# Optimization experiments

Hardware: AMD Instinct MI355X
Metric: run time of the kernel (lower is better)

## Reference

```python
import jax, jax.numpy as jnp
import numpy as np

T, H, I, E, Z, TOPK = 1024, 1024, 512, 32, 8, 4
ROUTED_SCALING = 1.0


def setup_inputs() -> dict:
    key = jax.random.key(0)
    k1, k2, k3, k4 = jax.random.split(key, 4)
    return {
        "hidden_states": jax.random.normal(k1, (T, H), jnp.float32),
        "router_w": jax.random.normal(k2, (E + Z, H), jnp.float32) * 0.02,
        "correction_bias": jnp.zeros((E + Z,), jnp.float32),
        "w_gate_up": jax.random.normal(k3, (E, 2 * I, H), jnp.float32) * 0.02,
        "w_down": jax.random.normal(k4, (E, H, I), jnp.float32) * 0.02,
        "top_k": TOPK,
    }


def reference(hidden_states, router_w, correction_bias, w_gate_up, w_down, top_k):
    # hidden_states: [T, H]; router_w: [E+Z, H]; w_gate_up: [E, 2I, H]; w_down: [E, H, I]
    t, h = hidden_states.shape
    e = w_gate_up.shape[0]
    i = w_down.shape[2]
    # --- router (float32, no bias; correction bias only affects selection) ---
    logits = jnp.einsum("th,eh->te", hidden_states.astype(jnp.float32), router_w)
    scores = jax.nn.softmax(logits, axis=-1)                     # [T, E+Z]
    _, idx = jax.lax.top_k(scores + correction_bias[None, :], top_k)  # [T, k]
    w = jnp.take_along_axis(scores, idx, axis=1) * ROUTED_SCALING     # renormalize=False
    # combine matrix [T, E+Z] (sparse top-k scattered dense)
    comb = jnp.zeros((t, scores.shape[1]), jnp.float32)
    comb = comb.at[jnp.arange(t)[:, None], idx].add(w)
    comb_routed = comb[:, :e].astype(hidden_states.dtype)        # [T, E]
    zero_w = comb[:, e:].sum(-1).astype(hidden_states.dtype)     # [T] identity zero-experts
    # --- grouped SiLU-gated expert MLPs (dense all-experts reference) ---
    gu = jnp.einsum("th,eih->eti", hidden_states, w_gate_up)     # [E, T, 2I]
    hmid = jax.nn.silu(gu[..., :i]) * gu[..., i:]                # [E, T, I]
    ye = jnp.einsum("eti,ehi->eth", hmid, w_down)                # [E, T, H]
    out = jnp.einsum("te,eth->th", comb_routed, ye)
    out = out + zero_w[:, None] * hidden_states
    return out
```

## Files before the change

kernel.cpp:

```cpp
#include <hip/hip_runtime.h>
#include <hip/hip_bf16.h>
#include <math.h>

#define TT   1024
#define HH   1024
#define II   512
#define EE   32
#define NE   40
#define TOPK 4
#define CAP  1024

#define GM  128
#define GNP 16
#define GK  32
#define KP  40
#define DN  32

typedef __attribute__((ext_vector_type(4))) short short4v;
typedef __attribute__((ext_vector_type(8))) short short8v;
typedef __attribute__((ext_vector_type(4))) float floatx4;

static __device__ __forceinline__ short f2bf(float f) {
    unsigned u = __float_as_uint(f);
    unsigned r = (u + 0x7fffu + ((u >> 16) & 1u)) >> 16;
    return (short)(r & 0xffffu);
}
static __device__ __forceinline__ float bf2f(short s) {
    return __uint_as_float(((unsigned)(unsigned short)s) << 16);
}
#if defined(__has_builtin)
#if __has_builtin(__builtin_amdgcn_cvt_pk_bf16_f32)
#define HAVE_PK_BF16 1
#endif
#endif
static __device__ __forceinline__ unsigned pk2(float a, float b) {
#ifdef HAVE_PK_BF16
    typedef __attribute__((ext_vector_type(2))) __bf16 bf2t;
    union { bf2t v; unsigned u; } cv;
    cv.v = __builtin_amdgcn_cvt_pk_bf16_f32(a, b);
    return cv.u;
#else
    return (unsigned)(unsigned short)f2bf(a) | ((unsigned)(unsigned short)f2bf(b) << 16);
#endif
}
static __device__ __forceinline__ short4v cvt4(float4 v) {
    union { unsigned u[2]; short4v s; } cv;
    cv.u[0] = pk2(v.x, v.y); cv.u[1] = pk2(v.z, v.w);
    return cv.s;
}

struct SMem {
    short As[GM * KP];
    short Bs[2 * GNP * KP];
    int   sl[GM];
    float wvs[GM];
};


__global__ __launch_bounds__(256, 4) void kA(
    const float* __restrict__ x, const float* __restrict__ rw,
    const float* __restrict__ bias, float* __restrict__ topk_w,
    float* __restrict__ zero_w, int* __restrict__ kexp,
    int* __restrict__ counts, int* __restrict__ slots, short* __restrict__ xb)
{
    const int bx = blockIdx.x, tid = threadIdx.x;
    const int lane = tid & 63;
    const int w    = tid >> 6;

    if (w < 2) {
        const int t = bx * 2 + w;
        float xv[16];
        #pragma unroll
        for (int i = 0; i < 16; ++i) xv[i] = x[(size_t)t * HH + 64 * i + lane];

        float mylogit = -INFINITY;
        for (int e0 = 0; e0 < NE; e0 += 4) {
            const float* r0 = rw + (size_t)e0 * HH;
            float p[4] = { 0.f, 0.f, 0.f, 0.f };
            #pragma unroll
            for (int i = 0; i < 16; ++i) {
                int h = 64 * i + lane;
                #pragma unroll
                for (int j = 0; j < 4; ++j) p[j] += xv[i] * r0[(size_t)j * HH + h];
            }
            #pragma unroll
            for (int j = 0; j < 4; ++j) {
                #pragma unroll
                for (int off = 32; off > 0; off >>= 1) p[j] += __shfl_xor(p[j], off);
                if (lane == e0 + j) mylogit = p[j];
            }
        }

        float m = mylogit;
        #pragma unroll
        for (int off = 32; off > 0; off >>= 1) m = fmaxf(m, __shfl_xor(m, off));
        float pexp = (lane < NE) ? expf(mylogit - m) : 0.f;
        float s = pexp;
        #pragma unroll
        for (int off = 32; off > 0; off >>= 1) s += __shfl_xor(s, off);
        const float score = pexp / s;

        float val = (lane < NE) ? score + bias[lane] : -INFINITY;
        int   kidx[TOPK];
        float kw[TOPK];
        #pragma unroll
        for (int k = 0; k < TOPK; ++k) {
            float v = val; int idx = lane;
            #pragma unroll
            for (int off = 32; off > 0; off >>= 1) {
                float ov = __shfl_xor(v, off);
                int   oi = __shfl_xor(idx, off);
                if (ov > v || (ov == v && oi < idx)) { v = ov; idx = oi; }
            }
            kidx[k] = idx;
            kw[k]   = __shfl(score, idx);
            if (lane == idx) val = -INFINITY;
        }

        if (lane == 0) {
            float zw = 0.f;
            #pragma unroll
            for (int k = 0; k < TOPK; ++k) {
                int slot = t * TOPK + k;
                topk_w[slot] = kw[k];
                kexp[slot]   = kidx[k];
                if (kidx[k] < EE) {
                    int pos = atomicAdd(&counts[kidx[k]], 1);
                    slots[kidx[k] * CAP + pos] = slot;
                } else {
                    zw += kw[k];
                }
            }
            zero_w[t] = zw;
        }
    } else {
        const int t = bx * 2 + (w - 2);
        const float4* xr = (const float4*)(x + (size_t)t * HH);
        short4v* xbr = (short4v*)(xb + (size_t)t * HH);
        #pragma unroll
        for (int i = 0; i < 4; ++i) xbr[lane + 64 * i] = cvt4(xr[lane + 64 * i]);
    }
}

__global__ __launch_bounds__(256, 4) void kB(
    const short* __restrict__ xb, const float* __restrict__ wgu,
    const int* __restrict__ counts, const int* __restrict__ slots,
    const float* __restrict__ topk_w, short* __restrict__ hmid)
{
    __shared__ SMem sm;
    const int bx = blockIdx.x, tid = threadIdx.x;
    const int e      = bx >> 5;
    const int c_base = (bx & 31) * GNP;
    const int cnt    = counts[e];
    const float* wb  = wgu + (size_t)e * (2 * II) * HH;

    const int lane = tid & 63;
    const int w    = tid >> 6;
    const int quad = lane >> 4;
    const int mcol = lane & 15;

    for (int m_base = 0; m_base < cnt; m_base += GM) {
        if (tid < GM) {
            int m = m_base + tid;
            int s = (m < cnt) ? slots[e * CAP + m] : -1;
            sm.sl[tid]  = s;
            sm.wvs[tid] = (s >= 0) ? topk_w[s] : 0.f;
        }
        __syncthreads();

        const int kcA = tid & 3;
        int rowA[2]; int slA[2]; const short* pA[2];
        #pragma unroll
        for (int it = 0; it < 2; ++it) {
            rowA[it] = (tid >> 2) + 64 * it;
            int s = sm.sl[rowA[it]];
            slA[it] = s;
            pA[it] = xb + (size_t)((s >= 0 ? s : 0) >> 2) * HH + kcA * 8;
        }
        const int kq   = tid & 7;
        const int rowB = tid >> 3;
        const int grow = (rowB < GNP) ? (c_base + rowB)
                                      : (II + c_base + (rowB - GNP));
        const float* pB = wb + (size_t)grow * HH + kq * 4;

        floatx4 accg[2] = {};
        floatx4 accu[2] = {};
        short8v pa[2]; float4 pb;
        const short8v szv = { 0,0,0,0,0,0,0,0 };

        #pragma unroll
        for (int it = 0; it < 2; ++it) pa[it] = (slA[it] >= 0) ? *(const short8v*)(pA[it]) : szv;
        pb = *(const float4*)(pB);

        for (int k0 = 0; k0 < HH; k0 += GK) {
            #pragma unroll
            for (int it = 0; it < 2; ++it) *(short8v*)&sm.As[rowA[it] * KP + kcA * 8] = pa[it];
            *(short4v*)&sm.Bs[rowB * KP + kq * 4] = cvt4(pb);
            __syncthreads();

            const int kn = k0 + GK;
            if (kn < HH) {
                #pragma unroll
                for (int it = 0; it < 2; ++it) pa[it] = (slA[it] >= 0) ? *(const short8v*)(pA[it] + kn) : szv;
                pb = *(const float4*)(pB + kn);
            }

            short8v a[2], bg, bu;
            #pragma unroll
            for (int i = 0; i < 2; ++i)
                a[i] = *(const short8v*)&sm.As[(w * 32 + i * 16 + mcol) * KP + quad * 8];
            bg = *(const short8v*)&sm.Bs[(mcol) * KP + quad * 8];
            bu = *(const short8v*)&sm.Bs[(GNP + mcol) * KP + quad * 8];
            #pragma unroll
            for (int i = 0; i < 2; ++i) {
                accg[i] = __builtin_amdgcn_mfma_f32_16x16x32_bf16(a[i], bg, accg[i], 0, 0, 0);
                accu[i] = __builtin_amdgcn_mfma_f32_16x16x32_bf16(a[i], bu, accu[i], 0, 0, 0);
            }
            __syncthreads();
        }

        #pragma unroll
        for (int i = 0; i < 2; ++i) {
            #pragma unroll
            for (int r = 0; r < 4; ++r) {
                int m = w * 32 + i * 16 + quad * 4 + r;
                int s = sm.sl[m];
                if (s < 0) continue;
                float g = accg[i][r], u = accu[i][r];
                float valf = sm.wvs[m] * g * u / (1.f + __expf(-g));
                hmid[(size_t)s * II + c_base + mcol] = f2bf(valf);
            }
        }
        __syncthreads();
    }
}

__global__ __launch_bounds__(256, 4) void kC(
    const short* __restrict__ hmid, const float* __restrict__ wd,
    const int* __restrict__ counts, const int* __restrict__ slots,
    short* __restrict__ ydown)
{
    __shared__ SMem sm;
    const int bx = blockIdx.x, tid = threadIdx.x;
    const int e      = bx >> 5;
    const int n_base = (bx & 31) * DN;
    const int cnt    = counts[e];
    const float* wb  = wd + (size_t)e * HH * II;

    const int lane = tid & 63;
    const int w    = tid >> 6;
    const int quad = lane >> 4;
    const int mcol = lane & 15;

    for (int m_base = 0; m_base < cnt; m_base += GM) {
        if (tid < GM) {
            int m = m_base + tid;
            sm.sl[tid] = (m < cnt) ? slots[e * CAP + m] : -1;
        }
        __syncthreads();

        const int kcA = tid & 3;
        int rowA[2]; int slA[2]; const short* pA[2];
        #pragma unroll
        for (int it = 0; it < 2; ++it) {
            rowA[it] = (tid >> 2) + 64 * it;
            int s = sm.sl[rowA[it]];
            slA[it] = s;
            pA[it] = hmid + (size_t)(s >= 0 ? s : 0) * II + kcA * 8;
        }
        const int kq   = tid & 7;
        const int rowB = tid >> 3;
        const float* pB = wb + (size_t)(n_base + rowB) * II + kq * 4;

        floatx4 acc[2][2] = {};
        short8v pa[2]; float4 pb;
        const short8v szv = { 0,0,0,0,0,0,0,0 };

        #pragma unroll
        for (int it = 0; it < 2; ++it) pa[it] = (slA[it] >= 0) ? *(const short8v*)(pA[it]) : szv;
        pb = *(const float4*)(pB);

        for (int k0 = 0; k0 < II; k0 += GK) {
            #pragma unroll
            for (int it = 0; it < 2; ++it) *(short8v*)&sm.As[rowA[it] * KP + kcA * 8] = pa[it];
            *(short4v*)&sm.Bs[rowB * KP + kq * 4] = cvt4(pb);
            __syncthreads();

            const int kn = k0 + GK;
            if (kn < II) {
                #pragma unroll
                for (int it = 0; it < 2; ++it) pa[it] = (slA[it] >= 0) ? *(const short8v*)(pA[it] + kn) : szv;
                pb = *(const float4*)(pB + kn);
            }

            short8v a[2], b[2];
            #pragma unroll
            for (int i = 0; i < 2; ++i)
                a[i] = *(const short8v*)&sm.As[(w * 32 + i * 16 + mcol) * KP + quad * 8];
            #pragma unroll
            for (int j = 0; j < 2; ++j)
                b[j] = *(const short8v*)&sm.Bs[(j * 16 + mcol) * KP + quad * 8];
            #pragma unroll
            for (int i = 0; i < 2; ++i)
                #pragma unroll
                for (int j = 0; j < 2; ++j)
                    acc[i][j] = __builtin_amdgcn_mfma_f32_16x16x32_bf16(a[i], b[j], acc[i][j], 0, 0, 0);
            __syncthreads();
        }

        #pragma unroll
        for (int i = 0; i < 2; ++i) {
            #pragma unroll
            for (int r = 0; r < 4; ++r) {
                int m = w * 32 + i * 16 + quad * 4 + r;
                int s = sm.sl[m];
                if (s < 0) continue;
                short* yrow = ydown + (size_t)s * HH + n_base;
                #pragma unroll
                for (int j = 0; j < 2; ++j)
                    yrow[j * 16 + mcol] = f2bf(acc[i][j][r]);
            }
        }
        __syncthreads();
    }
}

__global__ __launch_bounds__(256, 4) void kD(
    const float* __restrict__ x, const short* __restrict__ ydown,
    const int* __restrict__ kexp, const float* __restrict__ zero_w,
    float* __restrict__ out)
{
    const int bx = blockIdx.x, tid = threadIdx.x;
    const int t = bx;
    const float4 xvv = ((const float4*)(x + (size_t)t * HH))[tid];
    const float zw = zero_w[t];
    float4 o;
    o.x = zw * xvv.x; o.y = zw * xvv.y; o.z = zw * xvv.z; o.w = zw * xvv.w;
    #pragma unroll
    for (int k = 0; k < TOPK; ++k) {
        int slot = t * TOPK + k;
        if (kexp[slot] < EE) {
            short4v y = *(const short4v*)&ydown[(size_t)slot * HH + tid * 4];
            o.x += bf2f(y[0]); o.y += bf2f(y[1]);
            o.z += bf2f(y[2]); o.w += bf2f(y[3]);
        }
    }
    ((float4*)(out + (size_t)t * HH))[tid] = o;
}

extern "C" void kernel_launch(void* const* d_in, const int* in_sizes, int n_in,
                              void* d_out, int out_size, void* d_ws, size_t ws_size,
                              hipStream_t stream) {
    const float* x    = (const float*)d_in[0];
    const float* rw   = (const float*)d_in[1];
    const float* bias = (const float*)d_in[2];
    const float* wgu  = (const float*)d_in[3];
    const float* wd   = (const float*)d_in[4];
    float* out = (float*)d_out;

    char* ws = (char*)d_ws;
    int*   counts = (int*)ws;
    float* topk_w = (float*)(ws + 1024);
    float* zero_w = (float*)(ws + 17408);
    int*   kexp   = (int*)(ws + 21504);
    int*   slots  = (int*)(ws + 40960);
    short* xb     = (short*)(ws + 262144);
    short* hmid   = (short*)(ws + 2359296);
    short* ydown  = (short*)(ws + 6553600);

    hipMemsetAsync(counts, 0, EE * sizeof(int), stream);

    kA<<<dim3(512),  dim3(256), 0, stream>>>(x, rw, bias, topk_w, zero_w, kexp, counts, slots, xb);
    kB<<<dim3(1024), dim3(256), 0, stream>>>(xb, wgu, counts, slots, topk_w, hmid);
    kC<<<dim3(1024), dim3(256), 0, stream>>>(hmid, wd, counts, slots, ydown);
    kD<<<dim3(1024), dim3(256), 0, stream>>>(x, ydown, kexp, zero_w, out);
}
```

Before: 319.6 us.

## Load MFMA operands directly from global into registers and build slots deterministically

```diff
diff --git a/kernel.cpp b/kernel.cpp
--- a/kernel.cpp
+++ b/kernel.cpp
@@ -11,10 +11,7 @@
 #define CAP  1024
 
 #define GM  128
-#define GNP 16
 #define GK  32
-#define KP  40
-#define DN  32
 
 typedef __attribute__((ext_vector_type(4))) short short4v;
 typedef __attribute__((ext_vector_type(8))) short short8v;
@@ -48,20 +45,18 @@
     cv.u[0] = pk2(v.x, v.y); cv.u[1] = pk2(v.z, v.w);
     return cv.s;
 }
-
-struct SMem {
-    short As[GM * KP];
-    short Bs[2 * GNP * KP];
-    int   sl[GM];
-    float wvs[GM];
-};
+static __device__ __forceinline__ short8v pack8(float4 f0, float4 f1) {
+    union { short4v h[2]; short8v v; } u;
+    u.h[0] = cvt4(f0); u.h[1] = cvt4(f1);
+    return u.v;
+}
 
 
 __global__ __launch_bounds__(256, 4) void kA(
     const float* __restrict__ x, const float* __restrict__ rw,
     const float* __restrict__ bias, float* __restrict__ topk_w,
     float* __restrict__ zero_w, int* __restrict__ kexp,
-    int* __restrict__ counts, int* __restrict__ slots, short* __restrict__ xb)
+    short* __restrict__ xb)
 {
     const int bx = blockIdx.x, tid = threadIdx.x;
     const int lane = tid & 63;
@@ -124,12 +119,7 @@
                 int slot = t * TOPK + k;
                 topk_w[slot] = kw[k];
                 kexp[slot]   = kidx[k];
-                if (kidx[k] < EE) {
-                    int pos = atomicAdd(&counts[kidx[k]], 1);
-                    slots[kidx[k] * CAP + pos] = slot;
-                } else {
-                    zw += kw[k];
-                }
+                if (kidx[k] >= EE) zw += kw[k];
             }
             zero_w[t] = zw;
         }
@@ -142,15 +132,46 @@
     }
 }
 
-__global__ __launch_bounds__(256, 4) void kB(
+__global__ __launch_bounds__(256, 4) void kA2(
+    const int* __restrict__ kexp, int* __restrict__ counts,
+    int* __restrict__ slots)
+{
+    __shared__ int wsum[4];
+    __shared__ int base;
+    const int e = blockIdx.x;
+    const int tid = threadIdx.x, lane = tid & 63, w = tid >> 6;
+    if (tid == 0) base = 0;
+    __syncthreads();
+    for (int i0 = 0; i0 < TT * TOPK; i0 += 256) {
+        const int i = i0 + tid;
+        const bool m = (kexp[i] == e);
+        unsigned long long bal = __ballot(m);
+        int pre  = __popcll(bal & ((1ull << lane) - 1ull));
+        int wcnt = __popcll(bal);
+        if (lane == 0) wsum[w] = wcnt;
+        __syncthreads();
+        int woff = 0;
+        #pragma unroll
+        for (int j = 0; j < 4; ++j) if (j < w) woff += wsum[j];
+        const int tot = wsum[0] + wsum[1] + wsum[2] + wsum[3];
+        if (m) slots[e * CAP + base + woff + pre] = i;
+        __syncthreads();
+        if (tid == 0) base += tot;
+        __syncthreads();
+    }
+    if (tid == 0) counts[e] = base;
+}
+
+__global__ __launch_bounds__(256, 3) void kB(
     const short* __restrict__ xb, const float* __restrict__ wgu,
     const int* __restrict__ counts, const int* __restrict__ slots,
     const float* __restrict__ topk_w, short* __restrict__ hmid)
 {
-    __shared__ SMem sm;
+    __shared__ int   ssl[GM];
+    __shared__ float swv[GM];
     const int bx = blockIdx.x, tid = threadIdx.x;
     const int e      = bx >> 5;
-    const int c_base = (bx & 31) * GNP;
+    const int c_base = (bx & 31) * 16;
     const int cnt    = counts[e];
     const float* wb  = wgu + (size_t)e * (2 * II) * HH;
 
@@ -158,92 +179,134 @@
     const int w    = tid >> 6;
     const int quad = lane >> 4;
     const int mcol = lane & 15;
+    constexpr int NSLAB = HH / GK;
+
+    const float* pG = wb + (size_t)(c_base + mcol) * HH + quad * 8;
+    const float* pU = wb + (size_t)(II + c_base + mcol) * HH + quad * 8;
 
     for (int m_base = 0; m_base < cnt; m_base += GM) {
+        __syncthreads();
         if (tid < GM) {
             int m = m_base + tid;
             int s = (m < cnt) ? slots[e * CAP + m] : -1;
-            sm.sl[tid]  = s;
-            sm.wvs[tid] = (s >= 0) ? topk_w[s] : 0.f;
-        }
-        __syncthreads();
-
-        const int kcA = tid & 3;
-        int rowA[2]; int slA[2]; const short* pA[2];
-        #pragma unroll
-        for (int it = 0; it < 2; ++it) {
-            rowA[it] = (tid >> 2) + 64 * it;
-            int s = sm.sl[rowA[it]];
-            slA[it] = s;
-            pA[it] = xb + (size_t)((s >= 0 ? s : 0) >> 2) * HH + kcA * 8;
-        }
-        const int kq   = tid & 7;
-        const int rowB = tid >> 3;
-        const int grow = (rowB < GNP) ? (c_base + rowB)
-                                      : (II + c_base + (rowB - GNP));
-        const float* pB = wb + (size_t)grow * HH + kq * 4;
-
-        floatx4 accg[2] = {};
-        floatx4 accu[2] = {};
-        short8v pa[2]; float4 pb;
-        const short8v szv = { 0,0,0,0,0,0,0,0 };
-
-        #pragma unroll
-        for (int it = 0; it < 2; ++it) pa[it] = (slA[it] >= 0) ? *(const short8v*)(pA[it]) : szv;
-        pb = *(const float4*)(pB);
-
-        for (int k0 = 0; k0 < HH; k0 += GK) {
-            #pragma unroll
-            for (int it = 0; it < 2; ++it) *(short8v*)&sm.As[rowA[it] * KP + kcA * 8] = pa[it];
-            *(short4v*)&sm.Bs[rowB * KP + kq * 4] = cvt4(pb);
-            __syncthreads();
-
-            const int kn = k0 + GK;
-            if (kn < HH) {
-                #pragma unroll
-                for (int it = 0; it < 2; ++it) pa[it] = (slA[it] >= 0) ? *(const short8v*)(pA[it] + kn) : szv;
-                pb = *(const float4*)(pB + kn);
-            }
-
-            short8v a[2], bg, bu;
-            #pragma unroll
-            for (int i = 0; i < 2; ++i)
-                a[i] = *(const short8v*)&sm.As[(w * 32 + i * 16 + mcol) * KP + quad * 8];
-            bg = *(const short8v*)&sm.Bs[(mcol) * KP + quad * 8];
-            bu = *(const short8v*)&sm.Bs[(GNP + mcol) * KP + quad * 8];
-            #pragma unroll
-            for (int i = 0; i < 2; ++i) {
-                accg[i] = __builtin_amdgcn_mfma_f32_16x16x32_bf16(a[i], bg, accg[i], 0, 0, 0);
-                accu[i] = __builtin_amdgcn_mfma_f32_16x16x32_bf16(a[i], bu, accu[i], 0, 0, 0);
-            }
-            __syncthreads();
-        }
-
-        #pragma unroll
-        for (int i = 0; i < 2; ++i) {
-            #pragma unroll
-            for (int r = 0; r < 4; ++r) {
-                int m = w * 32 + i * 16 + quad * 4 + r;
-                int s = sm.sl[m];
-                if (s < 0) continue;
-                float g = accg[i][r], u = accu[i][r];
-                float valf = sm.wvs[m] * g * u / (1.f + __expf(-g));
-                hmid[(size_t)s * II + c_base + mcol] = f2bf(valf);
-            }
-        }
-        __syncthreads();
+            ssl[tid] = s;
+            swv[tid] = (s >= 0) ? topk_w[s] : 0.f;
+        }
+        __syncthreads();
+
+        const short *pA0, *pA1;
+        {
+            int s0 = ssl[w * 32 +      mcol];
+            int s1 = ssl[w * 32 + 16 + mcol];
+            pA0 = xb + (size_t)((s0 >= 0 ? s0 : 0) >> 2) * HH + quad * 8;
+            pA1 = xb + (size_t)((s1 >= 0 ? s1 : 0) >> 2) * HH + quad * 8;
+        }
+
+        floatx4 accg0 = {}, accg1 = {}, accu0 = {}, accu1 = {};
+
+        float4 g0_0,g1_0,u0_0,u1_0, g0_1,g1_1,u0_1,u1_1,
+               g0_2,g1_2,u0_2,u1_2, g0_3,g1_3,u0_3,u1_3;
+        short8v a0_0,a1_0, a0_1,a1_1;
+
+        g0_0=*(const float4*)(pG       ); g1_0=*(const float4*)(pG+4       );
+        u0_0=*(const float4*)(pU       ); u1_0=*(const float4*)(pU+4       );
+        g0_1=*(const float4*)(pG+GK    ); g1_1=*(const float4*)(pG+GK+4    );
+        u0_1=*(const float4*)(pU+GK    ); u1_1=*(const float4*)(pU+GK+4    );
+        g0_2=*(const float4*)(pG+2*GK  ); g1_2=*(const float4*)(pG+2*GK+4  );
+        u0_2=*(const float4*)(pU+2*GK  ); u1_2=*(const float4*)(pU+2*GK+4  );
+        g0_3=*(const float4*)(pG+3*GK  ); g1_3=*(const float4*)(pG+3*GK+4  );
+        u0_3=*(const float4*)(pU+3*GK  ); u1_3=*(const float4*)(pU+3*GK+4  );
+        a0_0=*(const short8v*)(pA0     ); a1_0=*(const short8v*)(pA1     );
+        a0_1=*(const short8v*)(pA0+GK  ); a1_1=*(const short8v*)(pA1+GK  );
+
+        for (int t = 0; t < NSLAB; t += 4) {
+            {
+                short8v bg = pack8(g0_0,g1_0), bu = pack8(u0_0,u1_0);
+                accg0 = __builtin_amdgcn_mfma_f32_16x16x32_bf16(a0_0, bg, accg0, 0, 0, 0);
+                accu0 = __builtin_amdgcn_mfma_f32_16x16x32_bf16(a0_0, bu, accu0, 0, 0, 0);
+                accg1 = __builtin_amdgcn_mfma_f32_16x16x32_bf16(a1_0, bg, accg1, 0, 0, 0);
+                accu1 = __builtin_amdgcn_mfma_f32_16x16x32_bf16(a1_0, bu, accu1, 0, 0, 0);
+                const int kb_ = (t + 4) * GK;
+                if (kb_ < HH) {
+                    g0_0=*(const float4*)(pG+kb_); g1_0=*(const float4*)(pG+kb_+4);
+                    u0_0=*(const float4*)(pU+kb_); u1_0=*(const float4*)(pU+kb_+4);
+                }
+                const int ka_ = (t + 2) * GK;
+                if (ka_ < HH) { a0_0=*(const short8v*)(pA0+ka_); a1_0=*(const short8v*)(pA1+ka_); }
+            }
+            {
+                short8v bg = pack8(g0_1,g1_1), bu = pack8(u0_1,u1_1);
+                accg0 = __builtin_amdgcn_mfma_f32_16x16x32_bf16(a0_1, bg, accg0, 0, 0, 0);
+                accu0 = __builtin_amdgcn_mfma_f32_16x16x32_bf16(a0_1, bu, accu0, 0, 0, 0);
+                accg1 = __builtin_amdgcn_mfma_f32_16x16x32_bf16(a1_1, bg, accg1, 0, 0, 0);
+                accu1 = __builtin_amdgcn_mfma_f32_16x16x32_bf16(a1_1, bu, accu1, 0, 0, 0);
+                const int kb_ = (t + 5) * GK;
+                if (kb_ < HH) {
+                    g0_1=*(const float4*)(pG+kb_); g1_1=*(const float4*)(pG+kb_+4);
+                    u0_1=*(const float4*)(pU+kb_); u1_1=*(const float4*)(pU+kb_+4);
+                }
+                const int ka_ = (t + 3) * GK;
+                if (ka_ < HH) { a0_1=*(const short8v*)(pA0+ka_); a1_1=*(const short8v*)(pA1+ka_); }
+            }
+            {
+                short8v bg = pack8(g0_2,g1_2), bu = pack8(u0_2,u1_2);
+                accg0 = __builtin_amdgcn_mfma_f32_16x16x32_bf16(a0_0, bg, accg0, 0, 0, 0);
+                accu0 = __builtin_amdgcn_mfma_f32_16x16x32_bf16(a0_0, bu, accu0, 0, 0, 0);
+                accg1 = __builtin_amdgcn_mfma_f32_16x16x32_bf16(a1_0, bg, accg1, 0, 0, 0);
+                accu1 = __builtin_amdgcn_mfma_f32_16x16x32_bf16(a1_0, bu, accu1, 0, 0, 0);
+                const int kb_ = (t + 6) * GK;
+                if (kb_ < HH) {
+                    g0_2=*(const float4*)(pG+kb_); g1_2=*(const float4*)(pG+kb_+4);
+                    u0_2=*(const float4*)(pU+kb_); u1_2=*(const float4*)(pU+kb_+4);
+                }
+                const int ka_ = (t + 4) * GK;
+                if (ka_ < HH) { a0_0=*(const short8v*)(pA0+ka_); a1_0=*(const short8v*)(pA1+ka_); }
+            }
+            {
+                short8v bg = pack8(g0_3,g1_3), bu = pack8(u0_3,u1_3);
+                accg0 = __builtin_amdgcn_mfma_f32_16x16x32_bf16(a0_1, bg, accg0, 0, 0, 0);
+                accu0 = __builtin_amdgcn_mfma_f32_16x16x32_bf16(a0_1, bu, accu0, 0, 0, 0);
+                accg1 = __builtin_amdgcn_mfma_f32_16x16x32_bf16(a1_1, bg, accg1, 0, 0, 0);
+                accu1 = __builtin_amdgcn_mfma_f32_16x16x32_bf16(a1_1, bu, accu1, 0, 0, 0);
+                const int kb_ = (t + 7) * GK;
+                if (kb_ < HH) {
+                    g0_3=*(const float4*)(pG+kb_); g1_3=*(const float4*)(pG+kb_+4);
+                    u0_3=*(const float4*)(pU+kb_); u1_3=*(const float4*)(pU+kb_+4);
+                }
+                const int ka_ = (t + 5) * GK;
+                if (ka_ < HH) { a0_1=*(const short8v*)(pA0+ka_); a1_1=*(const short8v*)(pA1+ka_); }
+            }
+        }
+
+        #pragma unroll
+        for (int r = 0; r < 4; ++r) {
+            int m0 = w * 32 + quad * 4 + r;
+            int s0 = ssl[m0];
+            if (s0 >= 0) {
+                float g = accg0[r], u = accu0[r];
+                hmid[(size_t)s0 * II + c_base + mcol] =
+                    f2bf(swv[m0] * g * u / (1.f + __expf(-g)));
+            }
+            int m1 = w * 32 + 16 + quad * 4 + r;
+            int s1 = ssl[m1];
+            if (s1 >= 0) {
+                float g = accg1[r], u = accu1[r];
+                hmid[(size_t)s1 * II + c_base + mcol] =
+                    f2bf(swv[m1] * g * u / (1.f + __expf(-g)));
+            }
+        }
     }
 }
 
-__global__ __launch_bounds__(256, 4) void kC(
+__global__ __launch_bounds__(256, 3) void kC(
     const short* __restrict__ hmid, const float* __restrict__ wd,
     const int* __restrict__ counts, const int* __restrict__ slots,
     short* __restrict__ ydown)
 {
-    __shared__ SMem sm;
+    __shared__ int ssl[GM];
     const int bx = blockIdx.x, tid = threadIdx.x;
     const int e      = bx >> 5;
-    const int n_base = (bx & 31) * DN;
+    const int n_base = (bx & 31) * 32;
     const int cnt    = counts[e];
     const float* wb  = wd + (size_t)e * HH * II;
 
@@ -251,77 +314,120 @@
     const int w    = tid >> 6;
     const int quad = lane >> 4;
     const int mcol = lane & 15;
+    constexpr int NSLAB = II / GK;
+
+    const float* pW0 = wb + (size_t)(n_base +      mcol) * II + quad * 8;
+    const float* pW1 = wb + (size_t)(n_base + 16 + mcol) * II + quad * 8;
 
     for (int m_base = 0; m_base < cnt; m_base += GM) {
+        __syncthreads();
         if (tid < GM) {
             int m = m_base + tid;
-            sm.sl[tid] = (m < cnt) ? slots[e * CAP + m] : -1;
-        }
-        __syncthreads();
-
-        const int kcA = tid & 3;
-        int rowA[2]; int slA[2]; const short* pA[2];
-        #pragma unroll
-        for (int it = 0; it < 2; ++it) {
-            rowA[it] = (tid >> 2) + 64 * it;
-            int s = sm.sl[rowA[it]];
-            slA[it] = s;
-            pA[it] = hmid + (size_t)(s >= 0 ? s : 0) * II + kcA * 8;
-        }
-        const int kq   = tid & 7;
-        const int rowB = tid >> 3;
-        const float* pB = wb + (size_t)(n_base + rowB) * II + kq * 4;
-
-        floatx4 acc[2][2] = {};
-        short8v pa[2]; float4 pb;
-        const short8v szv = { 0,0,0,0,0,0,0,0 };
-
-        #pragma unroll
-        for (int it = 0; it < 2; ++it) pa[it] = (slA[it] >= 0) ? *(const short8v*)(pA[it]) : szv;
-        pb = *(const float4*)(pB);
-
-        for (int k0 = 0; k0 < II; k0 += GK) {
-            #pragma unroll
-            for (int it = 0; it < 2; ++it) *(short8v*)&sm.As[rowA[it] * KP + kcA * 8] = pa[it];
-            *(short4v*)&sm.Bs[rowB * KP + kq * 4] = cvt4(pb);
-            __syncthreads();
-
-            const int kn = k0 + GK;
-            if (kn < II) {
-                #pragma unroll
-                for (int it = 0; it < 2; ++it) pa[it] = (slA[it] >= 0) ? *(const short8v*)(pA[it] + kn) : szv;
-                pb = *(const float4*)(pB + kn);
-            }
-
-            short8v a[2], b[2];
-            #pragma unroll
-            for (int i = 0; i < 2; ++i)
-                a[i] = *(const short8v*)&sm.As[(w * 32 + i * 16 + mcol) * KP + quad * 8];
-            #pragma unroll
-            for (int j = 0; j < 2; ++j)
-                b[j] = *(const short8v*)&sm.Bs[(j * 16 + mcol) * KP + quad * 8];
-            #pragma unroll
-            for (int i = 0; i < 2; ++i)
-                #pragma unroll
-                for (int j = 0; j < 2; ++j)
-                    acc[i][j] = __builtin_amdgcn_mfma_f32_16x16x32_bf16(a[i], b[j], acc[i][j], 0, 0, 0);
-            __syncthreads();
-        }
-
-        #pragma unroll
-        for (int i = 0; i < 2; ++i) {
-            #pragma unroll
-            for (int r = 0; r < 4; ++r) {
-                int m = w * 32 + i * 16 + quad * 4 + r;
-                int s = sm.sl[m];
-                if (s < 0) continue;
-                short* yrow = ydown + (size_t)s * HH + n_base;
-                #pragma unroll
-                for (int j = 0; j < 2; ++j)
-                    yrow[j * 16 + mcol] = f2bf(acc[i][j][r]);
-            }
-        }
-        __syncthreads();
+            ssl[tid] = (m < cnt) ? slots[e * CAP + m] : -1;
+        }
+        __syncthreads();
+
+        const short *pA0, *pA1;
+        {
+            int s0 = ssl[w * 32 +      mcol];
+            int s1 = ssl[w * 32 + 16 + mcol];
+            pA0 = hmid + (size_t)(s0 >= 0 ? s0 : 0) * II + quad * 8;
+            pA1 = hmid + (size_t)(s1 >= 0 ? s1 : 0) * II + quad * 8;
+        }
+
+        floatx4 acc00 = {}, acc01 = {}, acc10 = {}, acc11 = {};
+
+        float4 p0_0,p1_0,q0_0,q1_0, p0_1,p1_1,q0_1,q1_1,
+               p0_2,p1_2,q0_2,q1_2, p0_3,p1_3,q0_3,q1_3;
+        short8v a0_0,a1_0, a0_1,a1_1;
+
+        p0_0=*(const float4*)(pW0      ); p1_0=*(const float4*)(pW0+4      );
+        q0_0=*(const float4*)(pW1      ); q1_0=*(const float4*)(pW1+4      );
+        p0_1=*(const float4*)(pW0+GK   ); p1_1=*(const float4*)(pW0+GK+4   );
+        q0_1=*(const float4*)(pW1+GK   ); q1_1=*(const float4*)(pW1+GK+4   );
+        p0_2=*(const float4*)(pW0+2*GK ); p1_2=*(const float4*)(pW0+2*GK+4 );
+        q0_2=*(const float4*)(pW1+2*GK ); q1_2=*(const float4*)(pW1+2*GK+4 );
+        p0_3=*(const float4*)(pW0+3*GK ); p1_3=*(const float4*)(pW0+3*GK+4 );
+        q0_3=*(const float4*)(pW1+3*GK ); q1_3=*(const float4*)(pW1+3*GK+4 );
+        a0_0=*(const short8v*)(pA0     ); a1_0=*(const short8v*)(pA1     );
+        a0_1=*(const short8v*)(pA0+GK  ); a1_1=*(const short8v*)(pA1+GK  );
+
+        for (int t = 0; t < NSLAB; t += 4) {
+            {
+                short8v b0 = pack8(p0_0,p1_0), b1 = pack8(q0_0,q1_0);
+                acc00 = __builtin_amdgcn_mfma_f32_16x16x32_bf16(a0_0, b0, acc00, 0, 0, 0);
+                acc01 = __builtin_amdgcn_mfma_f32_16x16x32_bf16(a0_0, b1, acc01, 0, 0, 0);
+                acc10 = __builtin_amdgcn_mfma_f32_16x16x32_bf16(a1_0, b0, acc10, 0, 0, 0);
+                acc11 = __builtin_amdgcn_mfma_f32_16x16x32_bf16(a1_0, b1, acc11, 0, 0, 0);
+                const int kb_ = (t + 4) * GK;
+                if (kb_ < II) {
+                    p0_0=*(const float4*)(pW0+kb_); p1_0=*(const float4*)(pW0+kb_+4);
+                    q0_0=*(const float4*)(pW1+kb_); q1_0=*(const float4*)(pW1+kb_+4);
+                }
+                const int ka_ = (t + 2) * GK;
+                if (ka_ < II) { a0_0=*(const short8v*)(pA0+ka_); a1_0=*(const short8v*)(pA1+ka_); }
+            }
+            {
+                short8v b0 = pack8(p0_1,p1_1), b1 = pack8(q0_1,q1_1);
+                acc00 = __builtin_amdgcn_mfma_f32_16x16x32_bf16(a0_1, b0, acc00, 0, 0, 0);
+                acc01 = __builtin_amdgcn_mfma_f32_16x16x32_bf16(a0_1, b1, acc01, 0, 0, 0);
+                acc10 = __builtin_amdgcn_mfma_f32_16x16x32_bf16(a1_1, b0, acc10, 0, 0, 0);
+                acc11 = __builtin_amdgcn_mfma_f32_16x16x32_bf16(a1_1, b1, acc11, 0, 0, 0);
+                const int kb_ = (t + 5) * GK;
+                if (kb_ < II) {
+                    p0_1=*(const float4*)(pW0+kb_); p1_1=*(const float4*)(pW0+kb_+4);
+                    q0_1=*(const float4*)(pW1+kb_); q1_1=*(const float4*)(pW1+kb_+4);
+                }
+                const int ka_ = (t + 3) * GK;
+                if (ka_ < II) { a0_1=*(const short8v*)(pA0+ka_); a1_1=*(const short8v*)(pA1+ka_); }
+            }
+            {
+                short8v b0 = pack8(p0_2,p1_2), b1 = pack8(q0_2,q1_2);
+                acc00 = __builtin_amdgcn_mfma_f32_16x16x32_bf16(a0_0, b0, acc00, 0, 0, 0);
+                acc01 = __builtin_amdgcn_mfma_f32_16x16x32_bf16(a0_0, b1, acc01, 0, 0, 0);
+                acc10 = __builtin_amdgcn_mfma_f32_16x16x32_bf16(a1_0, b0, acc10, 0, 0, 0);
+                acc11 = __builtin_amdgcn_mfma_f32_16x16x32_bf16(a1_0, b1, acc11, 0, 0, 0);
+                const int kb_ = (t + 6) * GK;
+                if (kb_ < II) {
+                    p0_2=*(const float4*)(pW0+kb_); p1_2=*(const float4*)(pW0+kb_+4);
+                    q0_2=*(const float4*)(pW1+kb_); q1_2=*(const float4*)(pW1+kb_+4);
+                }
+                const int ka_ = (t + 4) * GK;
+                if (ka_ < II) { a0_0=*(const short8v*)(pA0+ka_); a1_0=*(const short8v*)(pA1+ka_); }
+            }
+            {
+                short8v b0 = pack8(p0_3,p1_3), b1 = pack8(q0_3,q1_3);
+                acc00 = __builtin_amdgcn_mfma_f32_16x16x32_bf16(a0_1, b0, acc00, 0, 0, 0);
+                acc01 = __builtin_amdgcn_mfma_f32_16x16x32_bf16(a0_1, b1, acc01, 0, 0, 0);
+                acc10 = __builtin_amdgcn_mfma_f32_16x16x32_bf16(a1_1, b0, acc10, 0, 0, 0);
+                acc11 = __builtin_amdgcn_mfma_f32_16x16x32_bf16(a1_1, b1, acc11, 0, 0, 0);
+                const int kb_ = (t + 7) * GK;
+                if (kb_ < II) {
+                    p0_3=*(const float4*)(pW0+kb_); p1_3=*(const float4*)(pW0+kb_+4);
+                    q0_3=*(const float4*)(pW1+kb_); q1_3=*(const float4*)(pW1+kb_+4);
+                }
+                const int ka_ = (t + 5) * GK;
+                if (ka_ < II) { a0_1=*(const short8v*)(pA0+ka_); a1_1=*(const short8v*)(pA1+ka_); }
+            }
+        }
+
+        #pragma unroll
+        for (int r = 0; r < 4; ++r) {
+            int m0 = w * 32 + quad * 4 + r;
+            int s0 = ssl[m0];
+            if (s0 >= 0) {
+                short* yrow = ydown + (size_t)s0 * HH + n_base;
+                yrow[mcol]      = f2bf(acc00[r]);
+                yrow[16 + mcol] = f2bf(acc01[r]);
+            }
+            int m1 = w * 32 + 16 + quad * 4 + r;
+            int s1 = ssl[m1];
+            if (s1 >= 0) {
+                short* yrow = ydown + (size_t)s1 * HH + n_base;
+                yrow[mcol]      = f2bf(acc10[r]);
+                yrow[16 + mcol] = f2bf(acc11[r]);
+            }
+        }
     }
 }
 
@@ -368,10 +474,9 @@
     short* hmid   = (short*)(ws + 2359296);
     short* ydown  = (short*)(ws + 6553600);
 
-    hipMemsetAsync(counts, 0, EE * sizeof(int), stream);
-
-    kA<<<dim3(512),  dim3(256), 0, stream>>>(x, rw, bias, topk_w, zero_w, kexp, counts, slots, xb);
-    kB<<<dim3(1024), dim3(256), 0, stream>>>(xb, wgu, counts, slots, topk_w, hmid);
-    kC<<<dim3(1024), dim3(256), 0, stream>>>(hmid, wd, counts, slots, ydown);
-    kD<<<dim3(1024), dim3(256), 0, stream>>>(x, ydown, kexp, zero_w, out);
-}
+    kA <<<dim3(512),  dim3(256), 0, stream>>>(x, rw, bias, topk_w, zero_w, kexp, xb);
+    kA2<<<dim3(32),   dim3(256), 0, stream>>>(kexp, counts, slots);
+    kB <<<dim3(1024), dim3(256), 0, stream>>>(xb, wgu, counts, slots, topk_w, hmid);
+    kC <<<dim3(1024), dim3(256), 0, stream>>>(hmid, wd, counts, slots, ydown);
+    kD <<<dim3(1024), dim3(256), 0, stream>>>(x, ydown, kexp, zero_w, out);
+}
```

Result: slower. 390.8 us (+22.3%).
